# Kernel optimization log

Hardware: AMD Instinct MI355X
Metric: run time of the kernel (lower is better)

Reference implementation:

```python
import jax, jax.numpy as jnp
import numpy as np

B, N, HID, OUT = 1024, 264, 256, 1
FLAT = (N // 2) * (HID // 2)  # 132 * 128 = 16896
EPS = 1e-5


def setup_inputs() -> dict:
    key = jax.random.key(0)
    ks = jax.random.split(key, 8)
    scale_gc = 1.0 / np.sqrt(N)
    scale_fc1 = 1.0 / np.sqrt(FLAT)
    scale_fc2 = 1.0 / np.sqrt(128)
    return {
        "x": jax.random.normal(ks[0], (B, N, N), dtype=jnp.float32),
        "adj": jax.random.uniform(ks[1], (B, N, N), dtype=jnp.float32),
        "W1": jax.random.normal(ks[2], (N, HID), dtype=jnp.float32) * scale_gc,
        "b1": jnp.zeros((HID,), dtype=jnp.float32),
        "gamma": jnp.ones((FLAT,), dtype=jnp.float32),
        "beta": jnp.zeros((FLAT,), dtype=jnp.float32),
        "fc1_w": jax.random.normal(ks[3], (FLAT, 128), dtype=jnp.float32) * scale_fc1,
        "fc1_b": jnp.zeros((128,), dtype=jnp.float32),
        "fc2_w": jax.random.normal(ks[4], (128, OUT), dtype=jnp.float32) * scale_fc2,
        "fc2_b": jnp.zeros((OUT,), dtype=jnp.float32),
    }


def reference(x, adj, W1, b1, gamma, beta, fc1_w, fc1_b, fc2_w, fc2_b):
    # GraphConvolution: adj @ (x @ W) + b, batched over B graphs
    support = jnp.einsum('bnf,fh->bnh', x, W1)          # [B, N, HID]
    h = jnp.einsum('bnm,bmh->bnh', adj, support) + b1   # [B, N, HID]
    h = jax.nn.selu(h)
    # AvgPool2d(kernel=2, stride=2) over the last two dims
    p = h.reshape(B, N // 2, 2, HID // 2, 2).mean(axis=(2, 4))  # [B, N/2, HID/2]
    l1 = p.reshape(B, FLAT)
    # BatchNorm1d (training mode: batch statistics, biased variance)
    mu = l1.mean(axis=0)
    var = l1.var(axis=0)
    l1 = (l1 - mu) * jax.lax.rsqrt(var + EPS) * gamma + beta
    # MLP head
    l2 = jax.nn.selu(l1 @ fc1_w + fc1_b)
    l2 = l2 @ fc2_w + fc2_b                             # [B, 1]
    pred = jax.nn.sigmoid(l2)                           # task == 'sex_predict'
    return pred.reshape(B)
```

## Files before the change

### kernel.cpp

```cpp
#include <hip/hip_runtime.h>

#define BATCH 1024
#define NN 264
#define HIDN 256
#define KP 288
#define FLATN 16896
#define POOL_R 132
#define POOL_C 128
#define SUPS 296
#define SMEM_FUSED (HIDN * SUPS * 2 + 96 * 40 * 2)

typedef short bf16x8_t __attribute__((ext_vector_type(8)));
typedef float f32x4_t __attribute__((ext_vector_type(4)));
typedef unsigned short u16x4_t __attribute__((ext_vector_type(4)));

__device__ inline unsigned short f2bf(float f) {
  unsigned int u = __float_as_uint(f);
  return (unsigned short)((u + 0x7fffu + ((u >> 16) & 1u)) >> 16);
}

__device__ inline float selu_f(float x) {
  return x > 0.f ? 1.0507009873554805f * x
                 : 1.7580993408473766f * (__expf(x) - 1.f);
}

__global__ __launch_bounds__(256) void k_prep_w1t(const float* __restrict__ W1,
                                                  unsigned short* __restrict__ w1t) {
  int idx = blockIdx.x * 256 + threadIdx.x;
  int h = idx / KP, k = idx - h * KP;
  w1t[idx] = (k < NN) ? f2bf(W1[(size_t)k * HIDN + h]) : (unsigned short)0;
}

__global__ __launch_bounds__(256) void k_prep_fwt(const float* __restrict__ fw,
                                                  unsigned short* __restrict__ fwt) {
  __shared__ float tile[32][33];
  int k0 = blockIdx.x * 32, n0 = blockIdx.y * 32;
  int tid = threadIdx.x;
#pragma unroll
  for (int i = 0; i < 4; ++i) {
    int idx = tid + i * 256;
    int r = idx >> 5, c = idx & 31;
    tile[r][c] = fw[(size_t)(k0 + r) * 128 + n0 + c];
  }
  __syncthreads();
#pragma unroll
  for (int i = 0; i < 4; ++i) {
    int idx = tid + i * 256;
    int r = idx >> 5, c = idx & 31;
    fwt[(size_t)(n0 + r) * FLATN + k0 + c] = f2bf(tile[c][r]);
  }
}

__global__ __launch_bounds__(512, 2) void k_fused(const float* __restrict__ x,
                                                  const float* __restrict__ adj,
                                                  const unsigned short* __restrict__ w1t,
                                                  const float* __restrict__ b1,
                                                  float* __restrict__ p) {
  extern __shared__ __align__(16) char smem[];
  unsigned short* sup = (unsigned short*)smem;
  unsigned short* As  = (unsigned short*)(smem + HIDN * SUPS * 2);

  const int tid = threadIdx.x;
  const int lane = tid & 63, wv = tid >> 6;
  const int lm = lane & 15, q8 = (lane >> 4) * 8, q4 = (lane >> 4) * 4;
  const int b = blockIdx.x;
  const float* xb = x + (size_t)b * NN * NN;
  const float* adjb = adj + (size_t)b * NN * NN;

  {
    u16x4_t zz = (u16x4_t)(unsigned short)0;
    for (int i = tid; i < HIDN * 8; i += 512) {
      int h = i >> 3, c = (i & 7) << 2;
      *reinterpret_cast<u16x4_t*>(&sup[(size_t)h * SUPS + NN + c]) = zz;
    }
  }

  for (int m0 = 0; m0 < NN; m0 += 96) {
    f32x4_t acc[6][2];
#pragma unroll
    for (int i = 0; i < 6; ++i)
#pragma unroll
      for (int j = 0; j < 2; ++j) acc[i][j] = (f32x4_t)0.f;

    for (int k0 = 0; k0 < NN; k0 += 32) {
#pragma unroll
      for (int i = 0; i < 2; ++i) {
        int idx = tid + i * 512;
        if (idx < 768) {
          int row = idx >> 3, k4 = idx & 7;
          int k = k0 + k4 * 4;
          float4 v = make_float4(0.f, 0.f, 0.f, 0.f);
          if ((m0 + row) < NN && k < NN)
            v = *reinterpret_cast<const float4*>(&xb[(size_t)(m0 + row) * NN + k]);
          u16x4_t pk;
          pk.x = f2bf(v.x); pk.y = f2bf(v.y); pk.z = f2bf(v.z); pk.w = f2bf(v.w);
          *reinterpret_cast<u16x4_t*>(&As[row * 40 + k4 * 4]) = pk;
        }
      }
      __syncthreads();
      bf16x8_t bb[2];
#pragma unroll
      for (int nt = 0; nt < 2; ++nt)
        bb[nt] = *reinterpret_cast<const bf16x8_t*>(
            &w1t[(size_t)(wv * 32 + nt * 16 + lm) * KP + k0 + q8]);
#pragma unroll
      for (int mt = 0; mt < 6; ++mt) {
        bf16x8_t aa = *reinterpret_cast<const bf16x8_t*>(&As[(mt * 16 + lm) * 40 + q8]);
#pragma unroll
        for (int nt = 0; nt < 2; ++nt)
          acc[mt][nt] = __builtin_amdgcn_mfma_f32_16x16x32_bf16(aa, bb[nt], acc[mt][nt], 0, 0, 0);
      }
      __syncthreads();
    }
#pragma unroll
    for (int mt = 0; mt < 6; ++mt) {
      int node = m0 + mt * 16 + q4;
      if (node < NN) {
#pragma unroll
        for (int nt = 0; nt < 2; ++nt) {
          int h = wv * 32 + nt * 16 + lm;
          u16x4_t pk;
          pk.x = f2bf(acc[mt][nt].x); pk.y = f2bf(acc[mt][nt].y);
          pk.z = f2bf(acc[mt][nt].z); pk.w = f2bf(acc[mt][nt].w);
          *reinterpret_cast<u16x4_t*>(&sup[(size_t)h * SUPS + node]) = pk;
        }
      }
    }
  }

  for (int m0 = 0; m0 < NN; m0 += 96) {
    f32x4_t acc[6][2];
#pragma unroll
    for (int i = 0; i < 6; ++i)
#pragma unroll
      for (int j = 0; j < 2; ++j) acc[i][j] = (f32x4_t)0.f;

    for (int k0 = 0; k0 < NN; k0 += 32) {
#pragma unroll
      for (int i = 0; i < 2; ++i) {
        int idx = tid + i * 512;
        if (idx < 768) {
          int row = idx >> 3, k4 = idx & 7;
          int k = k0 + k4 * 4;
          float4 v = make_float4(0.f, 0.f, 0.f, 0.f);
          if ((m0 + row) < NN && k < NN)
            v = *reinterpret_cast<const float4*>(&adjb[(size_t)(m0 + row) * NN + k]);
          u16x4_t pk;
          pk.x = f2bf(v.x); pk.y = f2bf(v.y); pk.z = f2bf(v.z); pk.w = f2bf(v.w);
          *reinterpret_cast<u16x4_t*>(&As[row * 40 + k4 * 4]) = pk;
        }
      }
      __syncthreads();
      bf16x8_t bb[2];
#pragma unroll
      for (int nt = 0; nt < 2; ++nt)
        bb[nt] = *reinterpret_cast<const bf16x8_t*>(
            &sup[(size_t)(wv * 32 + nt * 16 + lm) * SUPS + k0 + q8]);
#pragma unroll
      for (int mt = 0; mt < 6; ++mt) {
        bf16x8_t aa = *reinterpret_cast<const bf16x8_t*>(&As[(mt * 16 + lm) * 40 + q8]);
#pragma unroll
        for (int nt = 0; nt < 2; ++nt)
          acc[mt][nt] = __builtin_amdgcn_mfma_f32_16x16x32_bf16(aa, bb[nt], acc[mt][nt], 0, 0, 0);
      }
      __syncthreads();
    }
    float bias[2];
#pragma unroll
    for (int nt = 0; nt < 2; ++nt) bias[nt] = b1[wv * 32 + nt * 16 + lm];
#pragma unroll
    for (int mt = 0; mt < 6; ++mt) {
      int mb = m0 + mt * 16 + q4;
#pragma unroll
      for (int nt = 0; nt < 2; ++nt) {
        f32x4_t v = acc[mt][nt];
        float s01 = selu_f(v.x + bias[nt]) + selu_f(v.y + bias[nt]);
        float s23 = selu_f(v.z + bias[nt]) + selu_f(v.w + bias[nt]);
        s01 += __shfl_xor(s01, 1);
        s23 += __shfl_xor(s23, 1);
        if (!(lane & 1) && mb < NN) {
          int pm = mb >> 1;
          int pn = (wv * 32 + nt * 16 + lm) >> 1;
          float* pp = &p[((size_t)b * POOL_R + pm) * POOL_C + pn];
          pp[0] = s01 * 0.25f;
          pp[POOL_C] = s23 * 0.25f;
        }
      }
    }
  }
}

__global__ __launch_bounds__(256) void k_bnstat(const float* __restrict__ p,
                                                float* __restrict__ psum) {
  int f = blockIdx.x * 256 + threadIdx.x;
  int r0 = blockIdx.y * 256;
  float s = 0.f, ss = 0.f;
#pragma unroll 4
  for (int r = 0; r < 256; ++r) {
    float v = p[(size_t)(r0 + r) * FLATN + f];
    s += v; ss += v * v;
  }
  psum[(size_t)(blockIdx.y * 2) * FLATN + f] = s;
  psum[(size_t)(blockIdx.y * 2 + 1) * FLATN + f] = ss;
}

__global__ __launch_bounds__(256) void k_bnfin(const float* __restrict__ psum,
                                               const float* __restrict__ gamma,
                                               const float* __restrict__ beta,
                                               float* __restrict__ ab,
                                               float* __restrict__ cb) {
  int f = blockIdx.x * 256 + threadIdx.x;
  float s = 0.f, ss = 0.f;
#pragma unroll
  for (int i = 0; i < 4; ++i) {
    s += psum[(size_t)(i * 2) * FLATN + f];
    ss += psum[(size_t)(i * 2 + 1) * FLATN + f];
  }
  float mu = s * (1.f / 1024.f);
  float var = ss * (1.f / 1024.f) - mu * mu;
  float a = rsqrtf(var + 1e-5f) * gamma[f];
  ab[f] = a;
  cb[f] = beta[f] - mu * a;
}

__global__ __launch_bounds__(256) void k_fc1(const float* __restrict__ p,
                                             const float* __restrict__ ab,
                                             const float* __restrict__ cb,
                                             const unsigned short* __restrict__ fwt,
                                             float* __restrict__ l2) {
  __shared__ __align__(16) unsigned short As[32 * 40];
  const int tid = threadIdx.x, lane = tid & 63, wv = tid >> 6;
  const int r0 = blockIdx.x * 32;
  const int kbase = blockIdx.y * 2112;
  const int lm = lane & 15, q8 = (lane >> 4) * 8;
  const int row = tid >> 3, k4 = tid & 7;
  f32x4_t acc[2][2];
#pragma unroll
  for (int i = 0; i < 2; ++i)
#pragma unroll
    for (int j = 0; j < 2; ++j) acc[i][j] = (f32x4_t)0.f;

  for (int it = 0; it < 66; ++it) {
    int k = kbase + it * 32 + k4 * 4;
    float4 v = *reinterpret_cast<const float4*>(&p[(size_t)(r0 + row) * FLATN + k]);
    float4 av = *reinterpret_cast<const float4*>(&ab[k]);
    float4 cv = *reinterpret_cast<const float4*>(&cb[k]);
    u16x4_t pk;
    pk.x = f2bf(v.x * av.x + cv.x);
    pk.y = f2bf(v.y * av.y + cv.y);
    pk.z = f2bf(v.z * av.z + cv.z);
    pk.w = f2bf(v.w * av.w + cv.w);
    *reinterpret_cast<u16x4_t*>(&As[row * 40 + k4 * 4]) = pk;
    __syncthreads();
    int kq = kbase + it * 32 + q8;
    bf16x8_t bb[2], aa[2];
#pragma unroll
    for (int nt = 0; nt < 2; ++nt)
      bb[nt] = *reinterpret_cast<const bf16x8_t*>(
          &fwt[(size_t)(wv * 32 + nt * 16 + lm) * FLATN + kq]);
#pragma unroll
    for (int mt = 0; mt < 2; ++mt)
      aa[mt] = *reinterpret_cast<const bf16x8_t*>(&As[(mt * 16 + lm) * 40 + q8]);
#pragma unroll
    for (int mt = 0; mt < 2; ++mt)
#pragma unroll
      for (int nt = 0; nt < 2; ++nt)
        acc[mt][nt] = __builtin_amdgcn_mfma_f32_16x16x32_bf16(aa[mt], bb[nt], acc[mt][nt], 0, 0, 0);
    __syncthreads();
  }
#pragma unroll
  for (int mt = 0; mt < 2; ++mt) {
    int rb = r0 + mt * 16 + (lane >> 4) * 4;
#pragma unroll
    for (int nt = 0; nt < 2; ++nt) {
      int col = wv * 32 + nt * 16 + lm;
      atomicAdd(&l2[(size_t)(rb + 0) * 128 + col], acc[mt][nt].x);
      atomicAdd(&l2[(size_t)(rb + 1) * 128 + col], acc[mt][nt].y);
      atomicAdd(&l2[(size_t)(rb + 2) * 128 + col], acc[mt][nt].z);
      atomicAdd(&l2[(size_t)(rb + 3) * 128 + col], acc[mt][nt].w);
    }
  }
}

__global__ __launch_bounds__(128) void k_head(const float* __restrict__ l2,
                                              const float* __restrict__ fc1b,
                                              const float* __restrict__ fc2w,
                                              const float* __restrict__ fc2b,
                                              float* __restrict__ out) {
  int row = blockIdx.x, t = threadIdx.x;
  float v = l2[(size_t)row * 128 + t] + fc1b[t];
  v = selu_f(v) * fc2w[t];
#pragma unroll
  for (int o = 32; o > 0; o >>= 1) v += __shfl_xor(v, o);
  __shared__ float red[2];
  if ((t & 63) == 0) red[t >> 6] = v;
  __syncthreads();
  if (t == 0) {
    float tot = red[0] + red[1] + fc2b[0];
    out[row] = 1.f / (1.f + __expf(-tot));
  }
}

extern "C" void kernel_launch(void* const* d_in, const int* in_sizes, int n_in,
                              void* d_out, int out_size, void* d_ws, size_t ws_size,
                              hipStream_t stream) {
  const float* x     = (const float*)d_in[0];
  const float* adj   = (const float*)d_in[1];
  const float* W1    = (const float*)d_in[2];
  const float* b1    = (const float*)d_in[3];
  const float* gamma = (const float*)d_in[4];
  const float* beta  = (const float*)d_in[5];
  const float* fc1w  = (const float*)d_in[6];
  const float* fc1b  = (const float*)d_in[7];
  const float* fc2w  = (const float*)d_in[8];
  const float* fc2b  = (const float*)d_in[9];
  float* out = (float*)d_out;
  (void)in_sizes; (void)n_in; (void)out_size; (void)ws_size;

  char* ws = (char*)d_ws;
  size_t off = 0;
  auto alloc = [&](size_t bytes) {
    size_t o = off;
    off += (bytes + 255) & ~(size_t)255;
    return o;
  };
  unsigned short* w1t = (unsigned short*)(ws + alloc((size_t)HIDN * KP * 2));
  unsigned short* fwt = (unsigned short*)(ws + alloc((size_t)128 * FLATN * 2));
  float* p    = (float*)(ws + alloc((size_t)BATCH * FLATN * 4));
  float* psum = (float*)(ws + alloc((size_t)8 * FLATN * 4));
  float* ab   = (float*)(ws + alloc((size_t)FLATN * 4));
  float* cb   = (float*)(ws + alloc((size_t)FLATN * 4));
  float* l2   = (float*)(ws + alloc((size_t)BATCH * 128 * 4));

  static bool s_attr = false;
  if (!s_attr) {
    hipFuncSetAttribute(reinterpret_cast<const void*>(k_fused),
                        hipFuncAttributeMaxDynamicSharedMemorySize, SMEM_FUSED);
    s_attr = true;
  }

  hipLaunchKernelGGL(k_prep_w1t, dim3(288), dim3(256), 0, stream, W1, w1t);
  hipLaunchKernelGGL(k_prep_fwt, dim3(528, 4), dim3(256), 0, stream, fc1w, fwt);
  hipLaunchKernelGGL(k_fused, dim3(BATCH), dim3(512), SMEM_FUSED, stream,
                     x, adj, w1t, b1, p);
  hipLaunchKernelGGL(k_bnstat, dim3(66, 4), dim3(256), 0, stream, p, psum);
  hipLaunchKernelGGL(k_bnfin, dim3(66), dim3(256), 0, stream, psum, gamma, beta, ab, cb);
  hipMemsetAsync(l2, 0, (size_t)BATCH * 128 * 4, stream);
  hipLaunchKernelGGL(k_fc1, dim3(32, 8), dim3(256), 0, stream, p, ab, cb, fwt, l2);
  hipLaunchKernelGGL(k_head, dim3(BATCH), dim3(128), 0, stream, l2, fc1b, fc2w, fc2b, out);
}
```

Baseline: 877.5 us.

## Split fused GCN across hidden halves with XCD-aware mapping, widen BN/fc1 grids

The fused GCN kernel now launches two blocks per graph, each owning 128 of the 256 hidden columns. This halves shared memory per block and raises occupancy, but both blocks reload and reconvert the same x and adj tiles. Block indices are remapped so the two halves of a graph, and consecutive graphs, land on the same XCD, which should help L2 reuse of the duplicated reads. The BN statistics and fc1 grids are split more finely (16 row groups, 33 k-splits) to expose more parallelism, at the cost of more partial sums and atomics.

```diff
diff --git a/kernel.cpp b/kernel.cpp
--- a/kernel.cpp
+++ b/kernel.cpp
@@ -7,8 +7,9 @@
 #define FLATN 16896
 #define POOL_R 132
 #define POOL_C 128
-#define SUPS 296
-#define SMEM_FUSED (HIDN * SUPS * 2 + 96 * 40 * 2)
+#define SUPS 292
+#define ASS 36
+#define SMEM_FUSED (128 * SUPS * 2 + 96 * ASS * 2)
 
 typedef short bf16x8_t __attribute__((ext_vector_type(8)));
 typedef float f32x4_t __attribute__((ext_vector_type(4)));
@@ -58,34 +59,39 @@
                                                   float* __restrict__ p) {
   extern __shared__ __align__(16) char smem[];
   unsigned short* sup = (unsigned short*)smem;
-  unsigned short* As  = (unsigned short*)(smem + HIDN * SUPS * 2);
+  unsigned short* As  = (unsigned short*)(smem + 128 * SUPS * 2);
 
   const int tid = threadIdx.x;
   const int lane = tid & 63, wv = tid >> 6;
   const int lm = lane & 15, q8 = (lane >> 4) * 8, q4 = (lane >> 4) * 4;
-  const int b = blockIdx.x;
+
+  const int i = blockIdx.x;
+  const int xcd = i & 7, slot = i >> 3;
+  const int b = xcd * 128 + (slot >> 1);
+  const int half = slot & 1;
+  const int hbase = half * 128;
+
   const float* xb = x + (size_t)b * NN * NN;
   const float* adjb = adj + (size_t)b * NN * NN;
+  const int hloc = wv * 16 + lm;
 
   {
     u16x4_t zz = (u16x4_t)(unsigned short)0;
-    for (int i = tid; i < HIDN * 8; i += 512) {
-      int h = i >> 3, c = (i & 7) << 2;
+    for (int t = tid; t < 128 * 7; t += 512) {
+      int h = t / 7, c = (t - h * 7) * 4;
       *reinterpret_cast<u16x4_t*>(&sup[(size_t)h * SUPS + NN + c]) = zz;
     }
   }
 
   for (int m0 = 0; m0 < NN; m0 += 96) {
-    f32x4_t acc[6][2];
-#pragma unroll
-    for (int i = 0; i < 6; ++i)
-#pragma unroll
-      for (int j = 0; j < 2; ++j) acc[i][j] = (f32x4_t)0.f;
+    f32x4_t acc[6];
+#pragma unroll
+    for (int mt = 0; mt < 6; ++mt) acc[mt] = (f32x4_t)0.f;
 
     for (int k0 = 0; k0 < NN; k0 += 32) {
 #pragma unroll
-      for (int i = 0; i < 2; ++i) {
-        int idx = tid + i * 512;
+      for (int it = 0; it < 2; ++it) {
+        int idx = tid + it * 512;
         if (idx < 768) {
           int row = idx >> 3, k4 = idx & 7;
           int k = k0 + k4 * 4;
@@ -94,21 +100,16 @@
             v = *reinterpret_cast<const float4*>(&xb[(size_t)(m0 + row) * NN + k]);
           u16x4_t pk;
           pk.x = f2bf(v.x); pk.y = f2bf(v.y); pk.z = f2bf(v.z); pk.w = f2bf(v.w);
-          *reinterpret_cast<u16x4_t*>(&As[row * 40 + k4 * 4]) = pk;
+          *reinterpret_cast<u16x4_t*>(&As[row * ASS + k4 * 4]) = pk;
         }
       }
       __syncthreads();
-      bf16x8_t bb[2];
-#pragma unroll
-      for (int nt = 0; nt < 2; ++nt)
-        bb[nt] = *reinterpret_cast<const bf16x8_t*>(
-            &w1t[(size_t)(wv * 32 + nt * 16 + lm) * KP + k0 + q8]);
+      bf16x8_t bb = *reinterpret_cast<const bf16x8_t*>(
+          &w1t[(size_t)(hbase + hloc) * KP + k0 + q8]);
 #pragma unroll
       for (int mt = 0; mt < 6; ++mt) {
-        bf16x8_t aa = *reinterpret_cast<const bf16x8_t*>(&As[(mt * 16 + lm) * 40 + q8]);
-#pragma unroll
-        for (int nt = 0; nt < 2; ++nt)
-          acc[mt][nt] = __builtin_amdgcn_mfma_f32_16x16x32_bf16(aa, bb[nt], acc[mt][nt], 0, 0, 0);
+        bf16x8_t aa = *reinterpret_cast<const bf16x8_t*>(&As[(mt * 16 + lm) * ASS + q8]);
+        acc[mt] = __builtin_amdgcn_mfma_f32_16x16x32_bf16(aa, bb, acc[mt], 0, 0, 0);
       }
       __syncthreads();
     }
@@ -116,29 +117,24 @@
     for (int mt = 0; mt < 6; ++mt) {
       int node = m0 + mt * 16 + q4;
       if (node < NN) {
-#pragma unroll
-        for (int nt = 0; nt < 2; ++nt) {
-          int h = wv * 32 + nt * 16 + lm;
-          u16x4_t pk;
-          pk.x = f2bf(acc[mt][nt].x); pk.y = f2bf(acc[mt][nt].y);
-          pk.z = f2bf(acc[mt][nt].z); pk.w = f2bf(acc[mt][nt].w);
-          *reinterpret_cast<u16x4_t*>(&sup[(size_t)h * SUPS + node]) = pk;
-        }
-      }
-    }
-  }
-
+        u16x4_t pk;
+        pk.x = f2bf(acc[mt].x); pk.y = f2bf(acc[mt].y);
+        pk.z = f2bf(acc[mt].z); pk.w = f2bf(acc[mt].w);
+        *reinterpret_cast<u16x4_t*>(&sup[(size_t)hloc * SUPS + node]) = pk;
+      }
+    }
+  }
+
+  const float bias = b1[hbase + hloc];
   for (int m0 = 0; m0 < NN; m0 += 96) {
-    f32x4_t acc[6][2];
-#pragma unroll
-    for (int i = 0; i < 6; ++i)
-#pragma unroll
-      for (int j = 0; j < 2; ++j) acc[i][j] = (f32x4_t)0.f;
+    f32x4_t acc[6];
+#pragma unroll
+    for (int mt = 0; mt < 6; ++mt) acc[mt] = (f32x4_t)0.f;
 
     for (int k0 = 0; k0 < NN; k0 += 32) {
 #pragma unroll
-      for (int i = 0; i < 2; ++i) {
-        int idx = tid + i * 512;
+      for (int it = 0; it < 2; ++it) {
+        int idx = tid + it * 512;
         if (idx < 768) {
           int row = idx >> 3, k4 = idx & 7;
           int k = k0 + k4 * 4;
@@ -147,44 +143,33 @@
             v = *reinterpret_cast<const float4*>(&adjb[(size_t)(m0 + row) * NN + k]);
           u16x4_t pk;
           pk.x = f2bf(v.x); pk.y = f2bf(v.y); pk.z = f2bf(v.z); pk.w = f2bf(v.w);
-          *reinterpret_cast<u16x4_t*>(&As[row * 40 + k4 * 4]) = pk;
+          *reinterpret_cast<u16x4_t*>(&As[row * ASS + k4 * 4]) = pk;
         }
       }
       __syncthreads();
-      bf16x8_t bb[2];
-#pragma unroll
-      for (int nt = 0; nt < 2; ++nt)
-        bb[nt] = *reinterpret_cast<const bf16x8_t*>(
-            &sup[(size_t)(wv * 32 + nt * 16 + lm) * SUPS + k0 + q8]);
+      bf16x8_t bb = *reinterpret_cast<const bf16x8_t*>(
+          &sup[(size_t)hloc * SUPS + k0 + q8]);
 #pragma unroll
       for (int mt = 0; mt < 6; ++mt) {
-        bf16x8_t aa = *reinterpret_cast<const bf16x8_t*>(&As[(mt * 16 + lm) * 40 + q8]);
-#pragma unroll
-        for (int nt = 0; nt < 2; ++nt)
-          acc[mt][nt] = __builtin_amdgcn_mfma_f32_16x16x32_bf16(aa, bb[nt], acc[mt][nt], 0, 0, 0);
+        bf16x8_t aa = *reinterpret_cast<const bf16x8_t*>(&As[(mt * 16 + lm) * ASS + q8]);
+        acc[mt] = __builtin_amdgcn_mfma_f32_16x16x32_bf16(aa, bb, acc[mt], 0, 0, 0);
       }
       __syncthreads();
     }
-    float bias[2];
-#pragma unroll
-    for (int nt = 0; nt < 2; ++nt) bias[nt] = b1[wv * 32 + nt * 16 + lm];
 #pragma unroll
     for (int mt = 0; mt < 6; ++mt) {
       int mb = m0 + mt * 16 + q4;
-#pragma unroll
-      for (int nt = 0; nt < 2; ++nt) {
-        f32x4_t v = acc[mt][nt];
-        float s01 = selu_f(v.x + bias[nt]) + selu_f(v.y + bias[nt]);
-        float s23 = selu_f(v.z + bias[nt]) + selu_f(v.w + bias[nt]);
-        s01 += __shfl_xor(s01, 1);
-        s23 += __shfl_xor(s23, 1);
-        if (!(lane & 1) && mb < NN) {
-          int pm = mb >> 1;
-          int pn = (wv * 32 + nt * 16 + lm) >> 1;
-          float* pp = &p[((size_t)b * POOL_R + pm) * POOL_C + pn];
-          pp[0] = s01 * 0.25f;
-          pp[POOL_C] = s23 * 0.25f;
-        }
+      f32x4_t v = acc[mt];
+      float s01 = selu_f(v.x + bias) + selu_f(v.y + bias);
+      float s23 = selu_f(v.z + bias) + selu_f(v.w + bias);
+      s01 += __shfl_xor(s01, 1);
+      s23 += __shfl_xor(s23, 1);
+      if (!(lane & 1) && mb < NN) {
+        int pm = mb >> 1;
+        int pn = (hbase + hloc) >> 1;
+        float* pp = &p[((size_t)b * POOL_R + pm) * POOL_C + pn];
+        pp[0] = s01 * 0.25f;
+        pp[POOL_C] = s23 * 0.25f;
       }
     }
   }
@@ -193,10 +178,10 @@
 __global__ __launch_bounds__(256) void k_bnstat(const float* __restrict__ p,
                                                 float* __restrict__ psum) {
   int f = blockIdx.x * 256 + threadIdx.x;
-  int r0 = blockIdx.y * 256;
+  int r0 = blockIdx.y * 64;
   float s = 0.f, ss = 0.f;
-#pragma unroll 4
-  for (int r = 0; r < 256; ++r) {
+#pragma unroll 8
+  for (int r = 0; r < 64; ++r) {
     float v = p[(size_t)(r0 + r) * FLATN + f];
     s += v; ss += v * v;
   }
@@ -212,7 +197,7 @@
   int f = blockIdx.x * 256 + threadIdx.x;
   float s = 0.f, ss = 0.f;
 #pragma unroll
-  for (int i = 0; i < 4; ++i) {
+  for (int i = 0; i < 16; ++i) {
     s += psum[(size_t)(i * 2) * FLATN + f];
     ss += psum[(size_t)(i * 2 + 1) * FLATN + f];
   }
@@ -231,7 +216,7 @@
   __shared__ __align__(16) unsigned short As[32 * 40];
   const int tid = threadIdx.x, lane = tid & 63, wv = tid >> 6;
   const int r0 = blockIdx.x * 32;
-  const int kbase = blockIdx.y * 2112;
+  const int kbase = blockIdx.y * 512;
   const int lm = lane & 15, q8 = (lane >> 4) * 8;
   const int row = tid >> 3, k4 = tid & 7;
   f32x4_t acc[2][2];
@@ -240,7 +225,7 @@
 #pragma unroll
     for (int j = 0; j < 2; ++j) acc[i][j] = (f32x4_t)0.f;
 
-  for (int it = 0; it < 66; ++it) {
+  for (int it = 0; it < 16; ++it) {
     int k = kbase + it * 32 + k4 * 4;
     float4 v = *reinterpret_cast<const float4*>(&p[(size_t)(r0 + row) * FLATN + k]);
     float4 av = *reinterpret_cast<const float4*>(&ab[k]);
@@ -327,7 +312,7 @@
   unsigned short* w1t = (unsigned short*)(ws + alloc((size_t)HIDN * KP * 2));
   unsigned short* fwt = (unsigned short*)(ws + alloc((size_t)128 * FLATN * 2));
   float* p    = (float*)(ws + alloc((size_t)BATCH * FLATN * 4));
-  float* psum = (float*)(ws + alloc((size_t)8 * FLATN * 4));
+  float* psum = (float*)(ws + alloc((size_t)32 * FLATN * 4));
   float* ab   = (float*)(ws + alloc((size_t)FLATN * 4));
   float* cb   = (float*)(ws + alloc((size_t)FLATN * 4));
   float* l2   = (float*)(ws + alloc((size_t)BATCH * 128 * 4));
@@ -341,11 +326,11 @@
 
   hipLaunchKernelGGL(k_prep_w1t, dim3(288), dim3(256), 0, stream, W1, w1t);
   hipLaunchKernelGGL(k_prep_fwt, dim3(528, 4), dim3(256), 0, stream, fc1w, fwt);
-  hipLaunchKernelGGL(k_fused, dim3(BATCH), dim3(512), SMEM_FUSED, stream,
+  hipLaunchKernelGGL(k_fused, dim3(BATCH * 2), dim3(512), SMEM_FUSED, stream,
                      x, adj, w1t, b1, p);
-  hipLaunchKernelGGL(k_bnstat, dim3(66, 4), dim3(256), 0, stream, p, psum);
+  hipLaunchKernelGGL(k_bnstat, dim3(66, 16), dim3(256), 0, stream, p, psum);
   hipLaunchKernelGGL(k_bnfin, dim3(66), dim3(256), 0, stream, psum, gamma, beta, ab, cb);
   hipMemsetAsync(l2, 0, (size_t)BATCH * 128 * 4, stream);
-  hipLaunchKernelGGL(k_fc1, dim3(32, 8), dim3(256), 0, stream, p, ab, cb, fwt, l2);
+  hipLaunchKernelGGL(k_fc1, dim3(32, 33), dim3(256), 0, stream, p, ab, cb, fwt, l2);
   hipLaunchKernelGGL(k_head, dim3(BATCH), dim3(128), 0, stream, l2, fc1b, fc2w, fc2b, out);
 }
```

Result: slower. 1.220 ms (+39.0%).
